# Performance work log

Measured on AMD Instinct MI355X. Metric: run time of the kernel, lower is better.

The kernel has to match this reference:

```python
import jax, jax.numpy as jnp
import numpy as np

D = 1024      # in_features
H = 4096      # hidden_dims
E = 8         # expert_nums
K = 2         # top_k
B, S = 4, 2048


def setup_inputs() -> dict:
    key = jax.random.key(0)
    ks = jax.random.split(key, 8)
    def lin(k, fan_in, shape):
        bound = 1.0 / np.sqrt(fan_in)
        return jax.random.uniform(k, shape, jnp.float32, -bound, bound)
    return {
        "x":  jax.random.normal(ks[0], (B, S, D), jnp.float32),
        "Wg": lin(ks[1], D, (D, E)),
        "bg": lin(ks[2], D, (E,)),
        "W1": lin(ks[3], D, (E, D, H)),
        "b1": lin(ks[4], D, (E, H)),
        "W2": lin(ks[5], H, (E, H, D)),
        "b2": lin(ks[6], H, (E, D)),
    }


def reference(x, Wg, bg, W1, b1, W2, b2):
    B_, S_, D_ = x.shape
    xt = x.reshape(-1, D_)                                   # [N, D]
    # Router: softmax gating + top-k
    logits = xt @ Wg + bg                                    # [N, E]
    scores = jax.nn.softmax(logits, axis=-1)
    topk_probs, topk_idx = jax.lax.top_k(scores, K)          # [N, K]
    # Dense per-expert FFN (the source runs every expert on all tokens)
    h = jnp.einsum("nd,edh->enh", xt, W1) + b1[:, None, :]   # [E, N, H]
    h = jax.nn.gelu(h, approximate=False)
    eo = jnp.einsum("enh,ehd->end", h, W2) + b2[:, None, :]  # [E, N, D]
    # Gather selected experts per token and combine with gate weights
    eo = jnp.transpose(eo, (1, 0, 2))                        # [N, E, D]
    sel = jnp.take_along_axis(eo, topk_idx[:, :, None], axis=1)  # [N, K, D]
    out = jnp.einsum("nk,nkd->nd", topk_probs, sel)          # [N, D]
    return out.reshape(B_, S_, D_)
```

## Files before the change

### kernel.cpp

```cpp
#include <hip/hip_runtime.h>
#include <hip/hip_bf16.h>
#include <cstdint>
#include <cstddef>

using bf16 = __hip_bfloat16;
using short8 = __attribute__((ext_vector_type(8))) short;
using floatx4 = __attribute__((ext_vector_type(4))) float;

constexpr int D_IN = 1024;
constexpr int H_DIM = 4096;
constexpr int E_NUM = 8;
constexpr int NTOK = 8192;
constexpr int NPAIR = NTOK * 2;
constexpr int MAXTILES = 144;

constexpr size_t OFF_PTOK  = 1024;
constexpr size_t OFF_PPROB = 263168;
constexpr size_t OFF_SCHED = 525312;
constexpr size_t OFF_XBF   = 1048576;
constexpr size_t OFF_W2T   = OFF_XBF + (size_t)NTOK * D_IN * 2;
constexpr size_t OFF_HBUF  = OFF_W2T + (size_t)E_NUM * D_IN * H_DIM * 2;
constexpr size_t OFF_W1T   = OFF_HBUF + (size_t)NPAIR * H_DIM * 2;

__device__ __forceinline__ void cp16(const bf16* g, bf16* s) {
  __builtin_amdgcn_global_load_lds(
      (const __attribute__((address_space(1))) unsigned int*)g,
      (__attribute__((address_space(3))) unsigned int*)s, 16, 0, 0);
}

__global__ __launch_bounds__(256) void transpose_cvt(
    const float* __restrict__ in, bf16* __restrict__ out, int K, int N) {
  __shared__ float tile[64][65];
  const int e = blockIdx.z;
  const float* ip = in + (size_t)e * K * N + (size_t)(blockIdx.y * 64) * N + blockIdx.x * 64;
  bf16* op = out + (size_t)e * K * N + (size_t)(blockIdx.x * 64) * K + blockIdx.y * 64;
  const int tc = threadIdx.x & 15;
  const int tr = threadIdx.x >> 4;
#pragma unroll
  for (int r = 0; r < 4; r++) {
    const float4 v = *(const float4*)&ip[(size_t)(tr + r * 16) * N + tc * 4];
    *(float4*)&tile[tr + r * 16][tc * 4] = v;
  }
  __syncthreads();
  const int kg = threadIdx.x & 7;
  const int nb = threadIdx.x >> 3;
#pragma unroll
  for (int r = 0; r < 2; r++) {
    const int n = nb + r * 32;
    union { short8 v; bf16 h[8]; } u;
#pragma unroll
    for (int j = 0; j < 8; j++) u.h[j] = __float2bfloat16(tile[kg * 8 + j][n]);
    *(short8*)&op[(size_t)n * K + kg * 8] = u.v;
  }
}

__global__ __launch_bounds__(256) void router_kernel(
    const float* __restrict__ x, const float* __restrict__ Wg,
    const float* __restrict__ bg, bf16* __restrict__ Xbf,
    int* __restrict__ counts, int* __restrict__ pairTok, float* __restrict__ pairProb) {
  __shared__ int lcnt[E_NUM];
  __shared__ int sBase[E_NUM];
  __shared__ int sE0[32], sL0[32], sE1[32], sL1[32];
  __shared__ float sP0[32], sP1[32];
  const int lane = threadIdx.x & 63;
  const int wave = threadIdx.x >> 6;
  if (threadIdx.x < E_NUM) lcnt[threadIdx.x] = 0;
  __syncthreads();

  for (int tk = 0; tk < 8; tk++) {
    const int li = wave * 8 + tk;
    const int n = blockIdx.x * 32 + li;
    const float* xr = x + (size_t)n * D_IN;
    bf16* xbr = Xbf + (size_t)n * D_IN;
    float logit[E_NUM];
#pragma unroll
    for (int e = 0; e < E_NUM; e++) logit[e] = 0.f;
#pragma unroll
    for (int i = 0; i < 16; i++) {
      const int d = i * 64 + lane;
      const float xd = xr[d];
      xbr[d] = __float2bfloat16(xd);
      const float4* wr = (const float4*)(Wg + (size_t)d * E_NUM);
      const float4 w0 = wr[0], w1 = wr[1];
      logit[0] += xd * w0.x; logit[1] += xd * w0.y;
      logit[2] += xd * w0.z; logit[3] += xd * w0.w;
      logit[4] += xd * w1.x; logit[5] += xd * w1.y;
      logit[6] += xd * w1.z; logit[7] += xd * w1.w;
    }
#pragma unroll
    for (int e = 0; e < E_NUM; e++) {
#pragma unroll
      for (int off = 32; off >= 1; off >>= 1)
        logit[e] += __shfl_xor(logit[e], off, 64);
    }
    if (lane == 0) {
      float l[E_NUM], mx = -1e30f;
#pragma unroll
      for (int e = 0; e < E_NUM; e++) { l[e] = logit[e] + bg[e]; mx = fmaxf(mx, l[e]); }
      float ex[E_NUM], s = 0.f;
#pragma unroll
      for (int e = 0; e < E_NUM; e++) { ex[e] = expf(l[e] - mx); s += ex[e]; }
      int i0 = 0;
#pragma unroll
      for (int e = 1; e < E_NUM; e++) if (l[e] > l[i0]) i0 = e;
      int i1 = (i0 == 0) ? 1 : 0;
#pragma unroll
      for (int e = 0; e < E_NUM; e++) if (e != i0 && l[e] > l[i1]) i1 = e;
      const float inv = 1.f / s;
      sE0[li] = i0; sL0[li] = atomicAdd(&lcnt[i0], 1); sP0[li] = ex[i0] * inv;
      sE1[li] = i1; sL1[li] = atomicAdd(&lcnt[i1], 1); sP1[li] = ex[i1] * inv;
    }
  }
  __syncthreads();
  if (threadIdx.x < E_NUM)
    sBase[threadIdx.x] = atomicAdd(&counts[threadIdx.x], lcnt[threadIdx.x]);
  __syncthreads();
  if (threadIdx.x < 32) {
    const int li = threadIdx.x;
    const int n = blockIdx.x * 32 + li;
    const int e0 = sE0[li], p0 = sBase[e0] + sL0[li];
    pairTok[e0 * NTOK + p0] = n;
    pairProb[e0 * NTOK + p0] = sP0[li];
    const int e1 = sE1[li], p1 = sBase[e1] + sL1[li];
    pairTok[e1 * NTOK + p1] = n | (1 << 15);
    pairProb[e1 * NTOK + p1] = sP1[li];
  }
}

__global__ void sched_kernel(const int* __restrict__ counts, int* __restrict__ sched) {
  if (threadIdx.x == 0 && blockIdx.x == 0) {
    int* bases = sched;
    int* nTiles = sched + 8;
    int* tileMap = sched + 16;
    int base = 0, t = 0;
    for (int e = 0; e < E_NUM; e++) {
      bases[e] = base;
      const int nt = (counts[e] + 127) >> 7;
      for (int m = 0; m < nt; m++) tileMap[t++] = (e << 16) | m;
      base += counts[e];
    }
    *nTiles = t;
  }
}

template <int MODE, int K, int NC>
__global__ __launch_bounds__(256) void gemm_kernel(
    const bf16* __restrict__ A, const bf16* __restrict__ Wt,
    const float* __restrict__ bias, const int* __restrict__ counts,
    const int* __restrict__ pairTok, const float* __restrict__ pairProb,
    const int* __restrict__ sched, bf16* __restrict__ Hout, float* __restrict__ Rout) {
  const int tix = blockIdx.x % MAXTILES;
  const int nblk = blockIdx.x / MAXTILES;
  if (tix >= sched[8]) return;
  const int packed = sched[16 + tix];
  const int e = packed >> 16;
  const int m0 = (packed & 0xFFFF) * 128;
  const int cnt = counts[e];
  const int base = sched[e];
  const int n0 = nblk * 128;

  __shared__ __align__(16) bf16 As[128 * 32];
  __shared__ __align__(16) bf16 Bs[128 * 32];

  const int t = threadIdx.x;
  const int lane = t & 63;
  const int wave = t >> 6;
  const int wmq = wave >> 1, wnq = wave & 1;
  const int fr = lane & 15;
  const int kg = (lane >> 4) * 8;

  const bf16* aSrc[2];
  const bf16* bSrc[2];
#pragma unroll
  for (int i = 0; i < 2; i++) {
    const int lin = i * 256 + t;
    const int r = lin >> 2;
    const int c8 = (lin & 3) * 8;
    int p = m0 + r;
    if (p > cnt - 1) p = cnt - 1;
    if (MODE == 0) {
      const int tok = pairTok[e * NTOK + p] & 0x1FFF;
      aSrc[i] = A + (size_t)tok * K + c8;
    } else {
      aSrc[i] = A + (size_t)(base + p) * K + c8;
    }
    bSrc[i] = Wt + ((size_t)e * NC + n0 + r) * K + c8;
  }

  floatx4 acc[4][4];
#pragma unroll
  for (int ti = 0; ti < 4; ti++)
#pragma unroll
    for (int tj = 0; tj < 4; tj++)
      acc[ti][tj] = {0.f, 0.f, 0.f, 0.f};

  for (int k0 = 0; k0 < K; k0 += 32) {
#pragma unroll
    for (int i = 0; i < 2; i++) {
      cp16(aSrc[i] + k0, &As[(size_t)(i * 256 + t) * 8]);
      cp16(bSrc[i] + k0, &Bs[(size_t)(i * 256 + t) * 8]);
    }
    __syncthreads();
    short8 a[4], b[4];
#pragma unroll
    for (int ti = 0; ti < 4; ti++)
      a[ti] = *(const short8*)&As[(wmq * 64 + ti * 16 + fr) * 32 + kg];
#pragma unroll
    for (int tj = 0; tj < 4; tj++)
      b[tj] = *(const short8*)&Bs[(wnq * 64 + tj * 16 + fr) * 32 + kg];
#pragma unroll
    for (int ti = 0; ti < 4; ti++)
#pragma unroll
      for (int tj = 0; tj < 4; tj++)
        acc[ti][tj] = __builtin_amdgcn_mfma_f32_16x16x32_bf16(a[ti], b[tj], acc[ti][tj], 0, 0, 0);
    __syncthreads();
  }

  float bv[4];
#pragma unroll
  for (int tj = 0; tj < 4; tj++)
    bv[tj] = bias[(size_t)e * NC + n0 + wnq * 64 + tj * 16 + fr];

#pragma unroll
  for (int ti = 0; ti < 4; ti++) {
    const int rb = wmq * 64 + ti * 16 + (lane >> 4) * 4;
#pragma unroll
    for (int i = 0; i < 4; i++) {
      const int p = m0 + rb + i;
      if (p < cnt) {
        if (MODE == 0) {
          bf16* orow = Hout + (size_t)(base + p) * NC + n0 + wnq * 64 + fr;
#pragma unroll
          for (int tj = 0; tj < 4; tj++) {
            const float h = acc[ti][tj][i] + bv[tj];
            const float g = 0.5f * h * (1.f + erff(h * 0.70710678118f));
            orow[tj * 16] = __float2bfloat16(g);
          }
        } else {
          const int pt = pairTok[e * NTOK + p];
          const float pr = pairProb[e * NTOK + p];
          const int tok = pt & 0x1FFF, slot = (pt >> 15) & 1;
          float* orow = Rout + ((size_t)(tok * 2 + slot)) * NC + n0 + wnq * 64 + fr;
#pragma unroll
          for (int tj = 0; tj < 4; tj++)
            orow[tj * 16] = (acc[ti][tj][i] + bv[tj]) * pr;
        }
      }
    }
  }
}

__global__ __launch_bounds__(256) void combine_kernel(
    const float4* __restrict__ r, float4* __restrict__ o) {
  const int j = blockIdx.x * 256 + threadIdx.x;
  const int n = j >> 8, c = j & 255;
  const float4 a = r[(size_t)(n * 2) * 256 + c];
  const float4 b = r[(size_t)(n * 2 + 1) * 256 + c];
  o[j] = make_float4(a.x + b.x, a.y + b.y, a.z + b.z, a.w + b.w);
}

extern "C" void kernel_launch(void* const* d_in, const int* in_sizes, int n_in,
                              void* d_out, int out_size, void* d_ws, size_t ws_size,
                              hipStream_t stream) {
  const float* x  = (const float*)d_in[0];
  const float* Wg = (const float*)d_in[1];
  const float* bg = (const float*)d_in[2];
  const float* W1 = (const float*)d_in[3];
  const float* b1 = (const float*)d_in[4];
  const float* W2 = (const float*)d_in[5];
  const float* b2 = (const float*)d_in[6];
  float* out = (float*)d_out;
  char* ws = (char*)d_ws;

  int*   counts   = (int*)ws;
  int*   pairTok  = (int*)(ws + OFF_PTOK);
  float* pairProb = (float*)(ws + OFF_PPROB);
  int*   sched    = (int*)(ws + OFF_SCHED);
  bf16*  Xbf      = (bf16*)(ws + OFF_XBF);
  bf16*  W2t      = (bf16*)(ws + OFF_W2T);
  bf16*  Hbuf     = (bf16*)(ws + OFF_HBUF);
  bf16*  W1t      = (bf16*)(ws + OFF_W1T);
  float* resbuf   = (float*)W1t;

  hipMemsetAsync(counts, 0, 64, stream);
  transpose_cvt<<<dim3(H_DIM / 64, D_IN / 64, E_NUM), 256, 0, stream>>>(W1, W1t, D_IN, H_DIM);
  transpose_cvt<<<dim3(D_IN / 64, H_DIM / 64, E_NUM), 256, 0, stream>>>(W2, W2t, H_DIM, D_IN);
  router_kernel<<<NTOK / 32, 256, 0, stream>>>(x, Wg, bg, Xbf, counts, pairTok, pairProb);
  sched_kernel<<<1, 64, 0, stream>>>(counts, sched);
  gemm_kernel<0, D_IN, H_DIM><<<32 * MAXTILES, 256, 0, stream>>>(
      Xbf, W1t, b1, counts, pairTok, pairProb, sched, Hbuf, resbuf);
  gemm_kernel<1, H_DIM, D_IN><<<8 * MAXTILES, 256, 0, stream>>>(
      Hbuf, W2t, b2, counts, pairTok, pairProb, sched, Hbuf, resbuf);
  combine_kernel<<<(NTOK * D_IN / 4) / 256, 256, 0, stream>>>((const float4*)resbuf, (float4*)out);
}
```

Baseline: 842.0 us.

## Pipeline expert GEMMs with 3-stage LDS ring, swizzle, split-K atomics

Both expert GEMMs now use a 3-deep LDS ring buffer. Global-to-LDS loads for tile k+3 are issued while the current tile's MFMAs run, with explicit waitcnt/barrier control and an XOR swizzle meant to avoid LDS bank conflicts. The second GEMM is split-K in two and adds prob-weighted results into the zeroed output with float atomics, replacing the per-slot result buffer and the separate combine kernel. This aims to hide memory latency and drop a full pass over an intermediate buffer. In exchange it needs an output memset, makes float summation order nondeterministic, and prefetches past the end of the K range on the last iterations.

```diff
diff --git a/kernel.cpp b/kernel.cpp
--- a/kernel.cpp
+++ b/kernel.cpp
@@ -12,7 +12,7 @@
 constexpr int E_NUM = 8;
 constexpr int NTOK = 8192;
 constexpr int NPAIR = NTOK * 2;
-constexpr int MAXTILES = 144;
+constexpr int MAXT = 136;
 
 constexpr size_t OFF_PTOK  = 1024;
 constexpr size_t OFF_PPROB = 263168;
@@ -143,49 +143,54 @@
   }
 }
 
-template <int MODE, int K, int NC>
-__global__ __launch_bounds__(256) void gemm_kernel(
+template <int MODE, int K, int NC, int KS>
+__global__ __launch_bounds__(256, 3) void gemm_kernel(
     const bf16* __restrict__ A, const bf16* __restrict__ Wt,
     const float* __restrict__ bias, const int* __restrict__ counts,
     const int* __restrict__ pairTok, const float* __restrict__ pairProb,
-    const int* __restrict__ sched, bf16* __restrict__ Hout, float* __restrict__ Rout) {
-  const int tix = blockIdx.x % MAXTILES;
-  const int nblk = blockIdx.x / MAXTILES;
+    const int* __restrict__ sched, bf16* __restrict__ Hout, float* __restrict__ out) {
+  const int tix = blockIdx.x % MAXT;
+  int nb = blockIdx.x / MAXT;
   if (tix >= sched[8]) return;
+  int ks = 0;
+  if (MODE == 1) { ks = nb >> 3; nb &= 7; }
+  constexpr int KJOB = K / KS;
+  constexpr int NT = KJOB / 32;
+  const int ksOff = ks * KJOB;
+
   const int packed = sched[16 + tix];
   const int e = packed >> 16;
   const int m0 = (packed & 0xFFFF) * 128;
   const int cnt = counts[e];
   const int base = sched[e];
-  const int n0 = nblk * 128;
-
-  __shared__ __align__(16) bf16 As[128 * 32];
-  __shared__ __align__(16) bf16 Bs[128 * 32];
+  const int n0 = nb * 128;
+
+  __shared__ __align__(16) bf16 As[3 * 128 * 32];
+  __shared__ __align__(16) bf16 Bs[3 * 128 * 32];
 
   const int t = threadIdx.x;
   const int lane = t & 63;
   const int wave = t >> 6;
-  const int wmq = wave >> 1, wnq = wave & 1;
+  const int wm = wave >> 1, wn = wave & 1;
   const int fr = lane & 15;
-  const int kg = (lane >> 4) * 8;
-
-  const bf16* aSrc[2];
-  const bf16* bSrc[2];
-#pragma unroll
-  for (int i = 0; i < 2; i++) {
-    const int lin = i * 256 + t;
-    const int r = lin >> 2;
-    const int c8 = (lin & 3) * 8;
-    int p = m0 + r;
-    if (p > cnt - 1) p = cnt - 1;
-    if (MODE == 0) {
-      const int tok = pairTok[e * NTOK + p] & 0x1FFF;
-      aSrc[i] = A + (size_t)tok * K + c8;
-    } else {
-      aSrc[i] = A + (size_t)(base + p) * K + c8;
-    }
-    bSrc[i] = Wt + ((size_t)e * NC + n0 + r) * K + c8;
-  }
+  const int csel = ((lane >> 4) ^ (lane & 3)) << 3;
+  const int aBase = (wm * 64 + fr) * 32 + csel;
+  const int bBase = (wn * 64 + fr) * 32 + csel;
+
+  const int r0 = t >> 2, r1 = 64 + (t >> 2);
+  const int gc = (((t & 3) ^ (r0 & 3)) << 3);
+  int p0 = m0 + r0; if (p0 > cnt - 1) p0 = cnt - 1;
+  int p1 = m0 + r1; if (p1 > cnt - 1) p1 = cnt - 1;
+  const bf16 *aS0, *aS1;
+  if (MODE == 0) {
+    aS0 = A + (size_t)(pairTok[e * NTOK + p0] & 0x1FFF) * K + gc;
+    aS1 = A + (size_t)(pairTok[e * NTOK + p1] & 0x1FFF) * K + gc;
+  } else {
+    aS0 = A + (size_t)(base + p0) * K + ksOff + gc;
+    aS1 = A + (size_t)(base + p1) * K + ksOff + gc;
+  }
+  const bf16* bS0 = Wt + ((size_t)e * NC + n0 + r0) * K + ksOff + gc;
+  const bf16* bS1 = Wt + ((size_t)e * NC + n0 + r1) * K + ksOff + gc;
 
   floatx4 acc[4][4];
 #pragma unroll
@@ -194,42 +199,65 @@
     for (int tj = 0; tj < 4; tj++)
       acc[ti][tj] = {0.f, 0.f, 0.f, 0.f};
 
-  for (int k0 = 0; k0 < K; k0 += 32) {
-#pragma unroll
-    for (int i = 0; i < 2; i++) {
-      cp16(aSrc[i] + k0, &As[(size_t)(i * 256 + t) * 8]);
-      cp16(bSrc[i] + k0, &Bs[(size_t)(i * 256 + t) * 8]);
-    }
-    __syncthreads();
+#pragma unroll
+  for (int q = 0; q < 3; q++) {
+    cp16(aS0 + q * 32, &As[q * 4096 + t * 8]);
+    cp16(aS1 + q * 32, &As[q * 4096 + 2048 + t * 8]);
+    cp16(bS0 + q * 32, &Bs[q * 4096 + t * 8]);
+    cp16(bS1 + q * 32, &Bs[q * 4096 + 2048 + t * 8]);
+  }
+  asm volatile("s_waitcnt vmcnt(8)" ::: "memory");
+  __builtin_amdgcn_sched_barrier(0);
+  __builtin_amdgcn_s_barrier();
+  __builtin_amdgcn_sched_barrier(0);
+
+  int rb = 0;
+#pragma unroll 1
+  for (int kt = 0; kt < NT; kt++) {
     short8 a[4], b[4];
 #pragma unroll
-    for (int ti = 0; ti < 4; ti++)
-      a[ti] = *(const short8*)&As[(wmq * 64 + ti * 16 + fr) * 32 + kg];
-#pragma unroll
-    for (int tj = 0; tj < 4; tj++)
-      b[tj] = *(const short8*)&Bs[(wnq * 64 + tj * 16 + fr) * 32 + kg];
+    for (int i = 0; i < 4; i++) {
+      a[i] = *(const short8*)&As[rb + aBase + i * 512];
+      b[i] = *(const short8*)&Bs[rb + bBase + i * 512];
+    }
+    asm volatile("s_waitcnt lgkmcnt(0)" ::: "memory");
+    __builtin_amdgcn_sched_barrier(0);
+    __builtin_amdgcn_s_barrier();
+    __builtin_amdgcn_sched_barrier(0);
+    const int kq = (kt + 3) * 32;
+    cp16(aS0 + kq, &As[rb + t * 8]);
+    cp16(aS1 + kq, &As[rb + 2048 + t * 8]);
+    cp16(bS0 + kq, &Bs[rb + t * 8]);
+    cp16(bS1 + kq, &Bs[rb + 2048 + t * 8]);
+    __builtin_amdgcn_s_setprio(1);
 #pragma unroll
     for (int ti = 0; ti < 4; ti++)
 #pragma unroll
       for (int tj = 0; tj < 4; tj++)
         acc[ti][tj] = __builtin_amdgcn_mfma_f32_16x16x32_bf16(a[ti], b[tj], acc[ti][tj], 0, 0, 0);
-    __syncthreads();
+    __builtin_amdgcn_s_setprio(0);
+    asm volatile("s_waitcnt vmcnt(8)" ::: "memory");
+    __builtin_amdgcn_sched_barrier(0);
+    __builtin_amdgcn_s_barrier();
+    __builtin_amdgcn_sched_barrier(0);
+    rb += 4096;
+    if (rb == 12288) rb = 0;
   }
 
   float bv[4];
 #pragma unroll
   for (int tj = 0; tj < 4; tj++)
-    bv[tj] = bias[(size_t)e * NC + n0 + wnq * 64 + tj * 16 + fr];
+    bv[tj] = bias[(size_t)e * NC + n0 + wn * 64 + tj * 16 + fr];
 
 #pragma unroll
   for (int ti = 0; ti < 4; ti++) {
-    const int rb = wmq * 64 + ti * 16 + (lane >> 4) * 4;
+    const int rbrow = wm * 64 + ti * 16 + (lane >> 4) * 4;
 #pragma unroll
     for (int i = 0; i < 4; i++) {
-      const int p = m0 + rb + i;
+      const int p = m0 + rbrow + i;
       if (p < cnt) {
         if (MODE == 0) {
-          bf16* orow = Hout + (size_t)(base + p) * NC + n0 + wnq * 64 + fr;
+          bf16* orow = Hout + (size_t)(base + p) * NC + n0 + wn * 64 + fr;
 #pragma unroll
           for (int tj = 0; tj < 4; tj++) {
             const float h = acc[ti][tj][i] + bv[tj];
@@ -239,24 +267,18 @@
         } else {
           const int pt = pairTok[e * NTOK + p];
           const float pr = pairProb[e * NTOK + p];
-          const int tok = pt & 0x1FFF, slot = (pt >> 15) & 1;
-          float* orow = Rout + ((size_t)(tok * 2 + slot)) * NC + n0 + wnq * 64 + fr;
-#pragma unroll
-          for (int tj = 0; tj < 4; tj++)
-            orow[tj * 16] = (acc[ti][tj][i] + bv[tj]) * pr;
+          const int tok = pt & 0x1FFF;
+          float* orow = out + (size_t)tok * NC + n0 + wn * 64 + fr;
+#pragma unroll
+          for (int tj = 0; tj < 4; tj++) {
+            float v = acc[ti][tj][i];
+            if (ks == 0) v += bv[tj];
+            atomicAdd(&orow[tj * 16], v * pr);
+          }
         }
       }
     }
   }
-}
-
-__global__ __launch_bounds__(256) void combine_kernel(
-    const float4* __restrict__ r, float4* __restrict__ o) {
-  const int j = blockIdx.x * 256 + threadIdx.x;
-  const int n = j >> 8, c = j & 255;
-  const float4 a = r[(size_t)(n * 2) * 256 + c];
-  const float4 b = r[(size_t)(n * 2 + 1) * 256 + c];
-  o[j] = make_float4(a.x + b.x, a.y + b.y, a.z + b.z, a.w + b.w);
 }
 
 extern "C" void kernel_launch(void* const* d_in, const int* in_sizes, int n_in,
@@ -280,16 +302,15 @@
   bf16*  W2t      = (bf16*)(ws + OFF_W2T);
   bf16*  Hbuf     = (bf16*)(ws + OFF_HBUF);
   bf16*  W1t      = (bf16*)(ws + OFF_W1T);
-  float* resbuf   = (float*)W1t;
 
   hipMemsetAsync(counts, 0, 64, stream);
+  hipMemsetAsync(out, 0, (size_t)NTOK * D_IN * sizeof(float), stream);
   transpose_cvt<<<dim3(H_DIM / 64, D_IN / 64, E_NUM), 256, 0, stream>>>(W1, W1t, D_IN, H_DIM);
   transpose_cvt<<<dim3(D_IN / 64, H_DIM / 64, E_NUM), 256, 0, stream>>>(W2, W2t, H_DIM, D_IN);
   router_kernel<<<NTOK / 32, 256, 0, stream>>>(x, Wg, bg, Xbf, counts, pairTok, pairProb);
   sched_kernel<<<1, 64, 0, stream>>>(counts, sched);
-  gemm_kernel<0, D_IN, H_DIM><<<32 * MAXTILES, 256, 0, stream>>>(
-      Xbf, W1t, b1, counts, pairTok, pairProb, sched, Hbuf, resbuf);
-  gemm_kernel<1, H_DIM, D_IN><<<8 * MAXTILES, 256, 0, stream>>>(
-      Hbuf, W2t, b2, counts, pairTok, pairProb, sched, Hbuf, resbuf);
-  combine_kernel<<<(NTOK * D_IN / 4) / 256, 256, 0, stream>>>((const float4*)resbuf, (float4*)out);
-}
+  gemm_kernel<0, D_IN, H_DIM, 1><<<32 * MAXT, 256, 0, stream>>>(
+      Xbf, W1t, b1, counts, pairTok, pairProb, sched, Hbuf, nullptr);
+  gemm_kernel<1, H_DIM, D_IN, 2><<<16 * MAXT, 256, 0, stream>>>(
+      Hbuf, W2t, b2, counts, pairTok, pairProb, sched, nullptr, out);
+}
```

New measurement: 884.8 us. 5.1% more time.
